# Kernel optimization log

Measured on AMD Instinct MI355X. Metric: run time of the kernel, lower is better.

The kernel has to match this reference:

```python
import jax, jax.numpy as jnp
import numpy as np

B, T, C = 8, 2048, 1024
HS = 128           # head_size
N_TERMS = 2
THETA = 10000.0


def _rope_tables(dim, end):
    freqs = 1.0 / (THETA ** (jnp.arange(0, dim, 2, dtype=jnp.float32) / dim))  # [dim/2]
    ang = jnp.arange(end, dtype=jnp.float32)[:, None] * freqs[None, :]          # [end, dim/2]
    return jnp.cos(ang), jnp.sin(ang)


def _apply_rope(x, cos, sin):
    # x: [..., T, D]; pairs are interleaved (x0,x1),(x2,x3),...
    xr = x[..., 0::2]
    xi = x[..., 1::2]
    or_ = xr * cos - xi * sin
    oi = xr * sin + xi * cos
    return jnp.stack([or_, oi], axis=-1).reshape(x.shape)


def setup_inputs() -> dict:
    key = jax.random.key(0)
    ks = jax.random.split(key, 6)
    x = jax.random.normal(ks[0], (B, T, C), dtype=jnp.float32)
    Wq = jax.random.normal(ks[1], (N_TERMS, C, HS), dtype=jnp.float32) * 0.02
    Wk = jax.random.normal(ks[2], (N_TERMS, C, HS), dtype=jnp.float32) * 0.02
    Wv = jax.random.normal(ks[3], (C, 2 * HS), dtype=jnp.float32) * 0.02
    lambda_q = jax.random.normal(ks[4], (N_TERMS, HS), dtype=jnp.float32) * 0.1
    lambda_k = jax.random.normal(ks[5], (N_TERMS, HS), dtype=jnp.float32) * 0.1
    return {"x": x, "Wq": Wq, "Wk": Wk, "Wv": Wv,
            "lambda_q": lambda_q, "lambda_k": lambda_k, "layer_idx": 3}


def reference(x, Wq, Wk, Wv, lambda_q, lambda_k, layer_idx):
    Bx, Tx, Cx = x.shape
    n = Wq.shape[0]
    scale = 1.0 / (HS ** 0.5)

    v = x @ Wv                                   # [B,T,2*HS]
    q = jnp.einsum('btc,ncd->nbtd', x, Wq)       # [n,B,T,HS]
    k = jnp.einsum('btc,ncd->nbtd', x, Wk)

    cos, sin = _rope_tables(HS, Tx)              # [T, HS/2]
    q = _apply_rope(q, cos, sin)
    k = _apply_rope(k, cos, sin)

    att = jnp.einsum('nbtd,nbsd->nbts', q, k) * scale  # [n,B,T,T]
    causal = jnp.tril(jnp.ones((Tx, Tx), dtype=bool))
    att = jnp.where(causal, att, -jnp.inf)
    att = jax.nn.softmax(att, axis=-1)

    # lambda values
    lam_init = 0.8 - 0.6 * jnp.exp(-0.3 * (jnp.float32(layer_idx) - 1.0))
    e = jnp.mean(jnp.exp(lambda_q * lambda_k), axis=-1)         # [n]
    e_prev = jnp.concatenate([jnp.zeros((1,), e.dtype), e[:-1]])
    lam = e - e_prev + lam_init                                 # [n]
    signs = jnp.where(jnp.arange(n) % 2 == 1, -1.0, 1.0)

    diff_att = jnp.einsum('n,nbts->bts', signs * lam, att)      # [B,T,T]
    out = diff_att @ v                                          # [B,T,2*HS]
    return out
```

## Files before the change

### kernel.cpp

```cpp
#include <hip/hip_runtime.h>
#include <math.h>

#define B_DIM 8
#define T_DIM 2048
#define C_DIM 1024
#define HS_DIM 128
#define VD 256
#define M_DIM (B_DIM * T_DIM)
#define QK_ELEMS (M_DIM * HS_DIM)
#define SCALE 0.088388347648318447f
#define LOG_THETA 9.210340371976184f

#define QB_OFF   0u
#define KB_OFF   4194304u
#define VT_OFF   8388608u
#define WT_OFF   12582912u
#define XBH_OFF  13369344u
#define LAM_OFF  21757952u
#define XSPLIT_ELEMS 8388608u

typedef short s8v   __attribute__((ext_vector_type(8)));
typedef float f32x4 __attribute__((ext_vector_type(4)));
typedef float f32x16 __attribute__((ext_vector_type(16)));

__device__ __forceinline__ unsigned int bf16_rne(float f) {
    unsigned int u = __float_as_uint(f);
    return (u + 0x7fffu + ((u >> 16) & 1u)) >> 16;
}
__device__ __forceinline__ unsigned int pack_bf2(float lo, float hi) {
    return bf16_rne(lo) | (bf16_rne(hi) << 16);
}
__device__ __forceinline__ void async_cp16(const unsigned short* g, unsigned short* l) {
    __builtin_amdgcn_global_load_lds(
        (const __attribute__((address_space(1))) unsigned int*)g,
        (__attribute__((address_space(3))) unsigned int*)l, 16, 0, 0);
}

__global__ void lam_kernel(const float* __restrict__ lq, const float* __restrict__ lk,
                           const int* __restrict__ lidx, float* __restrict__ lam_out) {
    int t = threadIdx.x;
    float s0 = expf(lq[t] * lk[t]) + expf(lq[t + 64] * lk[t + 64]);
    float s1 = expf(lq[128 + t] * lk[128 + t]) + expf(lq[192 + t] * lk[192 + t]);
    #pragma unroll
    for (int off = 32; off > 0; off >>= 1) {
        s0 += __shfl_down(s0, off);
        s1 += __shfl_down(s1, off);
    }
    if (t == 0) {
        float e0 = s0 * (1.0f / 128.0f);
        float e1 = s1 * (1.0f / 128.0f);
        float li = 0.8f - 0.6f * expf(-0.3f * ((float)lidx[0] - 1.0f));
        lam_out[0] = e0 + li;
        lam_out[1] = -(e1 - e0 + li);
    }
}

__global__ __launch_bounds__(256) void cast_x_kernel(const float* __restrict__ x,
                                                     unsigned short* __restrict__ lo,
                                                     unsigned short* __restrict__ hi) {
    const size_t i8 = ((size_t)blockIdx.x * 256 + threadIdx.x) * 8;
    float4 a = *(const float4*)(x + i8);
    float4 b = *(const float4*)(x + i8 + 4);
    uint4 u;
    u.x = pack_bf2(a.x, a.y); u.y = pack_bf2(a.z, a.w);
    u.z = pack_bf2(b.x, b.y); u.w = pack_bf2(b.z, b.w);
    unsigned short* dst = (i8 < XSPLIT_ELEMS) ? (lo + i8) : (hi + (i8 - XSPLIT_ELEMS));
    *(uint4*)dst = u;
}

__global__ __launch_bounds__(256) void cast_wt_kernel(
    const float* __restrict__ Wq, const float* __restrict__ Wk,
    const float* __restrict__ Wv, unsigned short* __restrict__ wt) {
    __shared__ float tile[32][33];
    const int t = threadIdx.x;
    const int n0 = blockIdx.x * 32;
    const int k0 = blockIdx.y * 32;
    const int seg = n0 >> 7;
    const int nl = t & 31;
    const int ng = n0 + nl;
    const float* src; int ld;
    if (seg < 2)      { src = Wq + (size_t)seg * (C_DIM * HS_DIM) + (ng & 127); ld = 128; }
    else if (seg < 4) { src = Wk + (size_t)(seg - 2) * (C_DIM * HS_DIM) + (ng & 127); ld = 128; }
    else              { src = Wv + (ng - 512); ld = 256; }
    #pragma unroll
    for (int rep = 0; rep < 4; ++rep) {
        int kl = (t >> 5) + rep * 8;
        tile[kl][nl] = src[(size_t)(k0 + kl) * ld];
    }
    __syncthreads();
    unsigned int* wt32 = (unsigned int*)wt;
    #pragma unroll
    for (int rep = 0; rep < 2; ++rep) {
        int nl2 = (t >> 4) + rep * 16;
        int k2 = (t & 15) * 2;
        unsigned int u = pack_bf2(tile[k2][nl2], tile[k2 + 1][nl2]);
        wt32[((size_t)(n0 + nl2) * 1024 + k0 + k2) >> 1] = u;
    }
}

__global__ __launch_bounds__(256) void gemm_kernel(
    const unsigned short* __restrict__ xlo, const unsigned short* __restrict__ xhi,
    const unsigned short* __restrict__ wt,
    unsigned short* __restrict__ qo, unsigned short* __restrict__ ko,
    unsigned short* __restrict__ vo) {
    __shared__ unsigned short As[128 * 32];
    __shared__ unsigned short Bs[128 * 32];

    const int t = threadIdx.x;
    const int wv = t >> 6, lane = t & 63;
    const int quad = lane >> 4, l15 = lane & 15;
    const int m0 = blockIdx.x * 128;
    const int n0 = blockIdx.y * 128;
    const int wr = wv >> 1, wc = wv & 1;

    const unsigned short* xbase = (m0 < 8192)
        ? (xlo + (size_t)m0 * C_DIM) : (xhi + (size_t)(m0 - 8192) * C_DIM);

    f32x4 acc[4][4];
    #pragma unroll
    for (int i = 0; i < 4; ++i)
        #pragma unroll
        for (int j = 0; j < 4; ++j) acc[i][j] = (f32x4){0.f, 0.f, 0.f, 0.f};

    const int srow = lane >> 2;
    const int skof = (lane & 3) * 8;

    for (int k0 = 0; k0 < C_DIM; k0 += 32) {
        #pragma unroll
        for (int j = 0; j < 2; ++j) {
            const int c = wv * 2 + j;
            async_cp16(xbase + (size_t)(c * 16 + srow) * C_DIM + k0 + skof, As + c * 512);
        }
        #pragma unroll
        for (int j = 0; j < 2; ++j) {
            const int c = wv * 2 + j;
            async_cp16(wt + (size_t)(n0 + c * 16 + srow) * C_DIM + k0 + skof, Bs + c * 512);
        }
        __syncthreads();
        s8v af[4], bf[4];
        #pragma unroll
        for (int i = 0; i < 4; ++i)
            af[i] = *(const s8v*)&As[(wr * 64 + i * 16 + l15) * 32 + quad * 8];
        #pragma unroll
        for (int j = 0; j < 4; ++j)
            bf[j] = *(const s8v*)&Bs[(wc * 64 + j * 16 + l15) * 32 + quad * 8];
        #pragma unroll
        for (int i = 0; i < 4; ++i)
            #pragma unroll
            for (int j = 0; j < 4; ++j)
                acc[i][j] = __builtin_amdgcn_mfma_f32_16x16x32_bf16(af[i], bf[j], acc[i][j], 0, 0, 0);
        __syncthreads();
    }

    const int seg = n0 >> 7;
    if (seg < 4) {
        unsigned short* dstbuf = ((seg < 2) ? qo : ko) + (size_t)(seg & 1) * QK_ELEMS;
        float freqj[4];
        #pragma unroll
        for (int j = 0; j < 4; ++j) {
            const int d = wc * 64 + j * 16 + l15;
            freqj[j] = __expf((float)(d >> 1) * (-LOG_THETA / 64.f));
        }
        const int odd = lane & 1;
        #pragma unroll
        for (int i = 0; i < 4; ++i) {
            #pragma unroll
            for (int e = 0; e < 4; ++e) {
                const int m = m0 + wr * 64 + i * 16 + quad * 4 + e;
                const float trow = (float)(m & (T_DIM - 1));
                unsigned int* p32 = (unsigned int*)(dstbuf + (size_t)m * HS_DIM);
                #pragma unroll
                for (int j = 0; j < 4; ++j) {
                    const int d = wc * 64 + j * 16 + l15;
                    const float val = acc[i][j][e];
                    const float other = __shfl_xor(val, 1);
                    float sn_, cs_;
                    __sincosf(trow * freqj[j], &sn_, &cs_);
                    const float out = val * cs_ + (odd ? other * sn_ : -other * sn_);
                    const float out2 = __shfl_xor(out, 1);
                    if (!odd) p32[d >> 1] = pack_bf2(out, out2);
                }
            }
        }
    } else {
        const int bq = m0 >> 11;
        const int tbase = m0 & (T_DIM - 1);
        unsigned int* vT32 = (unsigned int*)vo;
        #pragma unroll
        for (int j = 0; j < 4; ++j) {
            const int d = (seg - 4) * 128 + wc * 64 + j * 16 + l15;
            const size_t rowbase = (size_t)(bq * VD + d) * (T_DIM / 2);
            #pragma unroll
            for (int i = 0; i < 4; ++i) {
                const int tok = tbase + wr * 64 + i * 16 + quad * 4;
                uint2 u;
                u.x = pack_bf2(acc[i][j][0], acc[i][j][1]);
                u.y = pack_bf2(acc[i][j][2], acc[i][j][3]);
                *(uint2*)&vT32[rowbase + (tok >> 1)] = u;
            }
        }
    }
}

#define KSTR 136
#define PSTR 72
#define OSTR 260
#define K_OFF 0
#define V_OFF 34816
#define P_OFF 67584
#define SM_TOTAL 76800

__global__ __launch_bounds__(256, 2) void attn_kernel(
    const unsigned short* __restrict__ qg, const unsigned short* __restrict__ kg,
    const unsigned short* __restrict__ vg, const float* __restrict__ lam,
    float* __restrict__ outp) {
    __shared__ __align__(16) unsigned char smem[SM_TOTAL];
    unsigned short* Ks = (unsigned short*)(smem + K_OFF);
    unsigned short* Vt = (unsigned short*)(smem + V_OFF);
    unsigned short* Ps = (unsigned short*)(smem + P_OFF);
    float* Ol = (float*)smem;
    float* Lsum = (float*)(smem + P_OFF);

    const int t = threadIdx.x;
    const int id = blockIdx.x;
    const int b = id & 7;
    const int sidx = id >> 3;
    const int strip = (sidx < 32) ? (63 - sidx) : (sidx - 32);
    const int q0 = strip * 32;
    const int nt = (strip >> 1) + 1;

    const int w = t >> 6, lane = t & 63;
    const int l31 = lane & 31, lh = lane >> 5;
    const int term = w & 1;
    const int kh = w >> 1;

    const float cn = lam[term];

    const unsigned short* qrow = qg
        + ((size_t)(term * B_DIM + b) * T_DIM + q0 + l31) * HS_DIM + lh * 8;
    s8v qa[8];
    #pragma unroll
    for (int ks = 0; ks < 8; ++ks)
        qa[ks] = *(const s8v*)(qrow + ks * 16);

    f32x16 o[4];
    #pragma unroll
    for (int dt = 0; dt < 4; ++dt)
        #pragma unroll
        for (int r = 0; r < 16; ++r) o[dt][r] = 0.f;
    float l_acc[16];
    #pragma unroll
    for (int r = 0; r < 16; ++r) l_acc[r] = 0.f;

    for (int it = 0; it < nt; ++it) {
        const int s0 = it * 64;
        #pragma unroll
        for (int rep = 0; rep < 8; ++rep) {
            int idx = t + rep * 256;
            int n = idx >> 10, rem = idx & 1023;
            int r = rem >> 4, seg = rem & 15;
            const uint4 g = *(const uint4*)(kg
                + ((size_t)(n * B_DIM + b) * T_DIM + s0 + r) * HS_DIM + seg * 8);
            *(uint4*)&Ks[(n * 64 + r) * KSTR + seg * 8] = g;
        }
        #pragma unroll
        for (int rep = 0; rep < 8; ++rep) {
            int idx = t + rep * 256;
            int d = idx >> 3, seg = idx & 7;
            const uint4 g = *(const uint4*)(vg
                + ((size_t)(b * VD + d) * T_DIM + s0) + seg * 8);
            *(uint4*)&Vt[d * 64 + ((seg ^ (d & 7)) * 8)] = g;
        }
        __syncthreads();

        f32x16 sc;
        #pragma unroll
        for (int r = 0; r < 16; ++r) sc[r] = 0.f;
        #pragma unroll
        for (int ks = 0; ks < 8; ++ks) {
            s8v kf = *(const s8v*)&Ks[(term * 64 + kh * 32 + l31) * KSTR
                                      + ks * 16 + lh * 8];
            sc = __builtin_amdgcn_mfma_f32_32x32x16_bf16(qa[ks], kf, sc, 0, 0, 0);
        }
        const int key = s0 + kh * 32 + l31;
        #pragma unroll
        for (int r = 0; r < 16; ++r) {
            const int row = (r & 3) + 8 * (r >> 2) + 4 * lh;
            const float p = (key <= q0 + row) ? __expf(sc[r] * SCALE) : 0.f;
            l_acc[r] += p;
            Ps[(term * 32 + row) * PSTR + kh * 32 + l31] = (unsigned short)bf16_rne(p);
        }
        __syncthreads();

        #pragma unroll
        for (int ks = 0; ks < 4; ++ks) {
            s8v pa = *(const s8v*)&Ps[(term * 32 + l31) * PSTR + ks * 16 + lh * 8];
            #pragma unroll
            for (int dt = 0; dt < 4; ++dt) {
                const int vrow = kh * 128 + dt * 32 + l31;
                s8v vb = *(const s8v*)&Vt[vrow * 64
                                          + (((ks * 2 + lh) ^ (l31 & 7)) * 8)];
                o[dt] = __builtin_amdgcn_mfma_f32_32x32x16_bf16(pa, vb, o[dt], 0, 0, 0);
            }
        }
        __syncthreads();
    }

    #pragma unroll
    for (int r = 0; r < 16; ++r) {
        float lt = l_acc[r];
        #pragma unroll
        for (int off = 1; off < 32; off <<= 1) lt += __shfl_xor(lt, off);
        if (l31 == 0) {
            const int row = (r & 3) + 8 * (r >> 2) + 4 * lh;
            Lsum[(term * 2 + kh) * 32 + row] = lt;
        }
    }
    __syncthreads();
    float inv[16];
    #pragma unroll
    for (int r = 0; r < 16; ++r) {
        const int row = (r & 3) + 8 * (r >> 2) + 4 * lh;
        inv[r] = cn / (Lsum[(term * 2 + 0) * 32 + row] + Lsum[(term * 2 + 1) * 32 + row]);
    }

    if (term) {
        #pragma unroll
        for (int dt = 0; dt < 4; ++dt)
            #pragma unroll
            for (int r = 0; r < 16; ++r) {
                const int row = (r & 3) + 8 * (r >> 2) + 4 * lh;
                Ol[row * OSTR + kh * 128 + dt * 32 + l31] = o[dt][r] * inv[r];
            }
    }
    __syncthreads();
    if (!term) {
        #pragma unroll
        for (int dt = 0; dt < 4; ++dt)
            #pragma unroll
            for (int r = 0; r < 16; ++r) {
                const int row = (r & 3) + 8 * (r >> 2) + 4 * lh;
                Ol[row * OSTR + kh * 128 + dt * 32 + l31] += o[dt][r] * inv[r];
            }
    }
    __syncthreads();
    #pragma unroll
    for (int rep = 0; rep < 8; ++rep) {
        int idx = t + rep * 256;
        int row = idx >> 6, c4 = idx & 63;
        float4 val = *(const float4*)&Ol[row * OSTR + c4 * 4];
        *(float4*)&outp[((size_t)(b * T_DIM + q0 + row)) * VD + c4 * 4] = val;
    }
}

extern "C" void kernel_launch(void* const* d_in, const int* in_sizes, int n_in,
                              void* d_out, int out_size, void* d_ws, size_t ws_size,
                              hipStream_t stream) {
    const float* x  = (const float*)d_in[0];
    const float* Wq = (const float*)d_in[1];
    const float* Wk = (const float*)d_in[2];
    const float* Wv = (const float*)d_in[3];
    const float* lq = (const float*)d_in[4];
    const float* lk = (const float*)d_in[5];
    const int* lidx = (const int*)d_in[6];

    unsigned short* ws = (unsigned short*)d_ws;
    unsigned short* qb   = ws + QB_OFF;
    unsigned short* kb   = ws + KB_OFF;
    unsigned short* vTb  = ws + VT_OFF;
    unsigned short* wtb  = ws + WT_OFF;
    unsigned short* xbhi = ws + XBH_OFF;
    float* lamb = (float*)(ws + LAM_OFF);
    unsigned short* xblo = (unsigned short*)d_out;
    (void)ws_size; (void)in_sizes; (void)n_in; (void)out_size;

    lam_kernel<<<dim3(1), dim3(64), 0, stream>>>(lq, lk, lidx, lamb);
    cast_x_kernel<<<dim3(8192), dim3(256), 0, stream>>>(x, xblo, xbhi);
    cast_wt_kernel<<<dim3(24, 32), dim3(256), 0, stream>>>(Wq, Wk, Wv, wtb);
    gemm_kernel<<<dim3(128, 6), dim3(256), 0, stream>>>(xblo, xbhi, wtb, qb, kb, vTb);
    attn_kernel<<<dim3(512), dim3(256), 0, stream>>>(qb, kb, vTb, lamb, (float*)d_out);
}
```

Baseline: 232.6 us.

## Double-buffer K/V tiles with async global-to-LDS copies in attention kernel

Replaces the synchronous register-staged K/V tile loads with asynchronous 16-byte global-to-LDS copies into two LDS buffers, prefetching tile it+1 while tile it is computed. The K layout switches from a padded stride to an XOR swizzle, the QK^T MFMA chain is split into two independent accumulators, and s_setprio is raised around the MFMA sections. The goal is to hide global load latency and cut the number of barriers per iteration. In exchange, LDS use roughly doubles and launch bounds drop to one block per CU, which lowers occupancy.

```diff
diff --git a/kernel.cpp b/kernel.cpp
--- a/kernel.cpp
+++ b/kernel.cpp
@@ -202,24 +202,20 @@
     }
 }
 
-#define KSTR 136
+#define BUFB 65536
+#define P_OFF 131072
 #define PSTR 72
 #define OSTR 260
-#define K_OFF 0
-#define V_OFF 34816
-#define P_OFF 67584
-#define SM_TOTAL 76800
-
-__global__ __launch_bounds__(256, 2) void attn_kernel(
+#define SM_TOTAL 140288
+
+__global__ __launch_bounds__(256, 1) void attn_kernel(
     const unsigned short* __restrict__ qg, const unsigned short* __restrict__ kg,
     const unsigned short* __restrict__ vg, const float* __restrict__ lam,
     float* __restrict__ outp) {
     __shared__ __align__(16) unsigned char smem[SM_TOTAL];
-    unsigned short* Ks = (unsigned short*)(smem + K_OFF);
-    unsigned short* Vt = (unsigned short*)(smem + V_OFF);
     unsigned short* Ps = (unsigned short*)(smem + P_OFF);
+    float* Lsum = (float*)(smem + P_OFF);
     float* Ol = (float*)smem;
-    float* Lsum = (float*)(smem + P_OFF);
 
     const int t = threadIdx.x;
     const int id = blockIdx.x;
@@ -243,6 +239,19 @@
     for (int ks = 0; ks < 8; ++ks)
         qa[ks] = *(const s8v*)(qrow + ks * 16);
 
+    const unsigned short* ksrc[8];
+    const unsigned short* vsrc[8];
+    #pragma unroll
+    for (int r = 0; r < 8; ++r) {
+        const int c = (r * 4 + w) * 64 + lane;
+        const int rowg = c >> 4, kslot = c & 15;
+        const int kterm = rowg >> 6, krow = rowg & 63;
+        ksrc[r] = kg + ((size_t)(kterm * B_DIM + b) * T_DIM + krow) * HS_DIM
+                     + (kslot ^ (krow & 7)) * 8;
+        const int dim = c >> 3, vslot = c & 7;
+        vsrc[r] = vg + ((size_t)(b * VD + dim)) * T_DIM + (vslot ^ (dim & 7)) * 8;
+    }
+
     f32x16 o[4];
     #pragma unroll
     for (int dt = 0; dt < 4; ++dt)
@@ -252,59 +261,78 @@
     #pragma unroll
     for (int r = 0; r < 16; ++r) l_acc[r] = 0.f;
 
+    {
+        unsigned short* kb = (unsigned short*)smem;
+        unsigned short* vb = (unsigned short*)(smem + 32768);
+        #pragma unroll
+        for (int r = 0; r < 8; ++r) {
+            async_cp16(ksrc[r], kb + (r * 4 + w) * 512);
+            async_cp16(vsrc[r], vb + (r * 4 + w) * 512);
+        }
+    }
+
     for (int it = 0; it < nt; ++it) {
         const int s0 = it * 64;
-        #pragma unroll
-        for (int rep = 0; rep < 8; ++rep) {
-            int idx = t + rep * 256;
-            int n = idx >> 10, rem = idx & 1023;
-            int r = rem >> 4, seg = rem & 15;
-            const uint4 g = *(const uint4*)(kg
-                + ((size_t)(n * B_DIM + b) * T_DIM + s0 + r) * HS_DIM + seg * 8);
-            *(uint4*)&Ks[(n * 64 + r) * KSTR + seg * 8] = g;
-        }
-        #pragma unroll
-        for (int rep = 0; rep < 8; ++rep) {
-            int idx = t + rep * 256;
-            int d = idx >> 3, seg = idx & 7;
-            const uint4 g = *(const uint4*)(vg
-                + ((size_t)(b * VD + d) * T_DIM + s0) + seg * 8);
-            *(uint4*)&Vt[d * 64 + ((seg ^ (d & 7)) * 8)] = g;
-        }
-        __syncthreads();
-
-        f32x16 sc;
-        #pragma unroll
-        for (int r = 0; r < 16; ++r) sc[r] = 0.f;
-        #pragma unroll
-        for (int ks = 0; ks < 8; ++ks) {
-            s8v kf = *(const s8v*)&Ks[(term * 64 + kh * 32 + l31) * KSTR
-                                      + ks * 16 + lh * 8];
-            sc = __builtin_amdgcn_mfma_f32_32x32x16_bf16(qa[ks], kf, sc, 0, 0, 0);
-        }
+        const unsigned short* Kb = (const unsigned short*)(smem + (it & 1) * BUFB);
+        const unsigned short* Vb = (const unsigned short*)(smem + (it & 1) * BUFB + 32768);
+
+        asm volatile("s_waitcnt vmcnt(0)" ::: "memory");
+        __builtin_amdgcn_s_barrier();
+
+        if (it + 1 < nt) {
+            const int sn = s0 + 64;
+            unsigned short* kb = (unsigned short*)(smem + ((it + 1) & 1) * BUFB);
+            unsigned short* vb = kb + 16384;
+            #pragma unroll
+            for (int r = 0; r < 8; ++r) {
+                async_cp16(ksrc[r] + (size_t)sn * HS_DIM, kb + (r * 4 + w) * 512);
+                async_cp16(vsrc[r] + sn, vb + (r * 4 + w) * 512);
+            }
+        }
+
+        f32x16 sc0, sc1;
+        #pragma unroll
+        for (int r = 0; r < 16; ++r) { sc0[r] = 0.f; sc1[r] = 0.f; }
+        const int krow = kh * 32 + l31;
+        __builtin_amdgcn_s_setprio(1);
+        #pragma unroll
+        for (int ks = 0; ks < 4; ++ks) {
+            s8v kf0 = *(const s8v*)&Kb[(term * 64 + krow) * 128
+                                       + ((ks * 2 + lh) ^ (l31 & 7)) * 8];
+            s8v kf1 = *(const s8v*)&Kb[(term * 64 + krow) * 128
+                                       + (((ks + 4) * 2 + lh) ^ (l31 & 7)) * 8];
+            sc0 = __builtin_amdgcn_mfma_f32_32x32x16_bf16(qa[ks], kf0, sc0, 0, 0, 0);
+            sc1 = __builtin_amdgcn_mfma_f32_32x32x16_bf16(qa[ks + 4], kf1, sc1, 0, 0, 0);
+        }
+        __builtin_amdgcn_s_setprio(0);
+        sc0 = sc0 + sc1;
+
         const int key = s0 + kh * 32 + l31;
         #pragma unroll
         for (int r = 0; r < 16; ++r) {
             const int row = (r & 3) + 8 * (r >> 2) + 4 * lh;
-            const float p = (key <= q0 + row) ? __expf(sc[r] * SCALE) : 0.f;
+            const float p = (key <= q0 + row) ? __expf(sc0[r] * SCALE) : 0.f;
             l_acc[r] += p;
             Ps[(term * 32 + row) * PSTR + kh * 32 + l31] = (unsigned short)bf16_rne(p);
         }
-        __syncthreads();
-
+        asm volatile("s_waitcnt lgkmcnt(0)" ::: "memory");
+        __builtin_amdgcn_s_barrier();
+
+        __builtin_amdgcn_s_setprio(1);
         #pragma unroll
         for (int ks = 0; ks < 4; ++ks) {
             s8v pa = *(const s8v*)&Ps[(term * 32 + l31) * PSTR + ks * 16 + lh * 8];
             #pragma unroll
             for (int dt = 0; dt < 4; ++dt) {
-                const int vrow = kh * 128 + dt * 32 + l31;
-                s8v vb = *(const s8v*)&Vt[vrow * 64
-                                          + (((ks * 2 + lh) ^ (l31 & 7)) * 8)];
+                const int dim = kh * 128 + dt * 32 + l31;
+                s8v vb = *(const s8v*)&Vb[dim * 64
+                                          + ((ks * 2 + lh) ^ (l31 & 7)) * 8];
                 o[dt] = __builtin_amdgcn_mfma_f32_32x32x16_bf16(pa, vb, o[dt], 0, 0, 0);
             }
         }
-        __syncthreads();
-    }
+        __builtin_amdgcn_s_setprio(0);
+    }
+    __syncthreads();
 
     #pragma unroll
     for (int r = 0; r < 16; ++r) {
```

After: 250.7 us. +7.8%, slower.
